# Kernel tuning notes

Measured on AMD Instinct MI355X. Metric: run time of the kernel, lower is better.

## Reference

```python
import jax, jax.numpy as jnp
import numpy as np

OUT_H, OUT_W = 7, 7
SPATIAL_SCALE = 0.25
SAMPLING_RATIO = 2


def setup_inputs() -> dict:
    key = jax.random.key(0)
    k1, k2, k3 = jax.random.split(key, 3)
    x = jax.random.normal(k1, (4, 256, 200, 200), dtype=jnp.float32)
    bidx = jax.random.randint(k2, (1024,), 0, 4).astype(jnp.float32)
    pts = jax.random.uniform(k3, (1024, 4), jnp.float32, 0.0, 800.0)
    x1 = jnp.minimum(pts[:, 0], pts[:, 2])
    x2 = jnp.maximum(pts[:, 0], pts[:, 2])
    y1 = jnp.minimum(pts[:, 1], pts[:, 3])
    y2 = jnp.maximum(pts[:, 1], pts[:, 3])
    rois = jnp.stack([bidx, x1, y1, x2, y2], axis=1)  # [B,5]
    return {"input": x, "rois": rois}


def reference(input, rois):
    feat = input                                  # [N,C,H,W]
    N, C, H, W = feat.shape
    B = rois.shape[0]
    S = SAMPLING_RATIO
    bi = rois[:, 0].astype(jnp.int32)             # [B] batch index (constant)
    boxes = rois[:, 1:] * SPATIAL_SCALE           # xyxy in feature coords
    rx1, ry1, rx2, ry2 = boxes[:, 0], boxes[:, 1], boxes[:, 2], boxes[:, 3]
    roi_w = jnp.maximum(rx2 - rx1, 1.0)
    roi_h = jnp.maximum(ry2 - ry1, 1.0)
    bin_h = roi_h / OUT_H                         # [B]
    bin_w = roi_w / OUT_W

    # per-ROI continuous sample coordinates: [B, OUT_H*S] and [B, OUT_W*S]
    off_h = (jnp.arange(OUT_H, dtype=jnp.float32)[:, None]
             + (jnp.arange(S, dtype=jnp.float32)[None, :] + 0.5) / S).reshape(-1)
    off_w = (jnp.arange(OUT_W, dtype=jnp.float32)[:, None]
             + (jnp.arange(S, dtype=jnp.float32)[None, :] + 0.5) / S).reshape(-1)
    ys = ry1[:, None] + off_h[None, :] * bin_h[:, None]   # [B, Hs]
    xs = rx1[:, None] + off_w[None, :] * bin_w[:, None]   # [B, Ws]

    # bilinear sampling; pixel i's value sits at continuous coordinate i+0.5
    # (this is the "alignment" handled inside point_interpolate)
    py = jnp.clip(ys - 0.5, 0.0, float(H - 1))
    px = jnp.clip(xs - 0.5, 0.0, float(W - 1))
    y0 = jnp.floor(py).astype(jnp.int32)
    x0 = jnp.floor(px).astype(jnp.int32)
    y1i = jnp.minimum(y0 + 1, H - 1)
    x1i = jnp.minimum(x0 + 1, W - 1)
    wy = (py - y0.astype(py.dtype))[:, :, None, None]     # [B,Hs,1,1]
    wx = (px - x0.astype(px.dtype))[:, None, :, None]     # [B,1,Ws,1]

    b = bi[:, None, None]

    def gather(yy, xx):
        # advanced indexing -> [B, Hs, Ws, C]
        return feat[b, :, yy[:, :, None], xx[:, None, :]]

    v = (gather(y0, x0) * (1.0 - wy) * (1.0 - wx)
         + gather(y0, x1i) * (1.0 - wy) * wx
         + gather(y1i, x0) * wy * (1.0 - wx)
         + gather(y1i, x1i) * wy * wx)                    # [B,Hs,Ws,C]

    # average pool the S x S samples within each output bin
    out = v.reshape(B, OUT_H, S, OUT_W, S, C).mean(axis=(2, 4))  # [B,OH,OW,C]
    return out.transpose(0, 3, 1, 2)                             # [B,C,OH,OW]
```

## Files before the change

kernel.cpp:

```cpp
#include <hip/hip_runtime.h>
#include <hip/hip_bf16.h>

#define CC 256
#define HH 200
#define WW 200
#define PLANE (HH * WW)
#define OUT_H 7
#define OUT_W 7
#define NSP   (OUT_H * OUT_W)
#define BMAX  1024

__global__ __launch_bounds__(256) void nchw2nhwc_bf16_sort(
    const float* __restrict__ in, __hip_bfloat16* __restrict__ out,
    const float* __restrict__ rois, int B, unsigned short* __restrict__ perm)
{
    __shared__ float tile[64][65];
    __shared__ unsigned skey[BMAX];

    int n  = blockIdx.z;
    int c0 = blockIdx.y * 64;
    int p0 = blockIdx.x * 64;
    int tx = threadIdx.x & 63;
    int ty = threadIdx.x >> 6;

    const float* src = in + ((size_t)n * CC + c0) * PLANE + p0;
    #pragma unroll
    for (int i = 0; i < 16; ++i) {
        int c = i * 4 + ty;
        tile[c][tx] = src[(size_t)c * PLANE + tx];
    }
    __syncthreads();
    __hip_bfloat16* dst = out + ((size_t)n * PLANE + p0) * CC + c0;
    #pragma unroll
    for (int i = 0; i < 16; ++i) {
        int p = i * 4 + ty;
        dst[(size_t)p * CC + tx] = __float2bfloat16(tile[tx][p]);
    }

    if (blockIdx.x == 0 && blockIdx.y == 0 && blockIdx.z == 0) {
        int t = threadIdx.x;
        for (int i = t; i < BMAX; i += 256) {
            unsigned k = 0xFFFFFFFFu;
            if (i < B) {
                const float* r = rois + i * 5;
                unsigned bi = (unsigned)(int)r[0];
                float cx = (r[1] + r[3]) * 0.125f;
                float cy = (r[2] + r[4]) * 0.125f;
                unsigned ix = (unsigned)fminf(fmaxf(cx, 0.f), 255.f);
                unsigned iy = (unsigned)fminf(fmaxf(cy, 0.f), 255.f);
                unsigned m = 0;
                #pragma unroll
                for (int bp = 0; bp < 8; ++bp) {
                    m |= ((ix >> bp) & 1u) << (2 * bp);
                    m |= ((iy >> bp) & 1u) << (2 * bp + 1);
                }
                k = (bi << 26) | (m << 10) | (unsigned)i;
            }
            skey[i] = k;
        }
        __syncthreads();
        for (int size = 2; size <= BMAX; size <<= 1) {
            for (int stride = size >> 1; stride > 0; stride >>= 1) {
                for (int i = t; i < BMAX; i += 256) {
                    int p = i ^ stride;
                    if (p > i) {
                        bool up = ((i & size) == 0);
                        unsigned a = skey[i], b2 = skey[p];
                        if ((a > b2) == up) { skey[i] = b2; skey[p] = a; }
                    }
                }
                __syncthreads();
            }
        }
        for (int i = t; i < BMAX; i += 256) perm[i] = (unsigned short)(skey[i] & 1023u);
    }
}

__global__ __launch_bounds__(256) void roialign_nhwc2_bf16s(
    const __hip_bfloat16* __restrict__ nhwc,
    const float* __restrict__ rois,
    const unsigned short* __restrict__ perm,
    float* __restrict__ out)
{
    __shared__ float obuf[128 * NSP];
    int nblk = gridDim.x;
    int bid  = blockIdx.x;
    int pos;
    if ((nblk & 7) == 0) { int cpx = nblk >> 3; pos = (bid & 7) * cpx + (bid >> 3); }
    else                 { pos = bid; }
    int slot = pos >> 1;
    int cg   = pos & 1;
    int b    = (int)perm[slot];

    int t  = threadIdx.x;
    int q  = t & 63;
    int wv = t >> 6;

    const float* r = rois + b * 5;
    int   bi  = (int)r[0];
    float rx1 = r[1] * 0.25f, ry1 = r[2] * 0.25f;
    float rx2 = r[3] * 0.25f, ry2 = r[4] * 0.25f;
    float bin_w = fmaxf(rx2 - rx1, 1.0f) * (1.0f / OUT_W);
    float bin_h = fmaxf(ry2 - ry1, 1.0f) * (1.0f / OUT_H);

    const __hip_bfloat16* base = nhwc + (size_t)bi * PLANE * CC + cg * 128 + 2 * q;

    int s0 = wv * 13;
    #pragma unroll
    for (int k = 0; k < 13; ++k) {
        unsigned s = (unsigned)min(s0 + k, NSP - 1);
        unsigned ph = s / 7u, pw = s % 7u;
        float a0 = 0.f, a1 = 0.f;
        #pragma unroll
        for (int iy = 0; iy < 2; ++iy) {
            float yy = ry1 + ((float)ph + ((float)iy + 0.5f) * 0.5f) * bin_h;
            float py = fminf(fmaxf(yy - 0.5f, 0.0f), (float)(HH - 1));
            int   y0 = min((int)py, HH - 2);
            float fy = py - (float)y0;
            #pragma unroll
            for (int ix = 0; ix < 2; ++ix) {
                float xx = rx1 + ((float)pw + ((float)ix + 0.5f) * 0.5f) * bin_w;
                float px = fminf(fmaxf(xx - 0.5f, 0.0f), (float)(WW - 1));
                int   x0 = min((int)px, WW - 2);
                float fx = px - (float)x0;

                const __hip_bfloat16* p00 = base + (size_t)(y0 * WW + x0) * CC;
                unsigned u00 = *(const unsigned*)(p00);
                unsigned u01 = *(const unsigned*)(p00 + CC);
                unsigned u10 = *(const unsigned*)(p00 + WW * CC);
                unsigned u11 = *(const unsigned*)(p00 + WW * CC + CC);

                float w00 = (1.f - fy) * (1.f - fx);
                float w01 = (1.f - fy) * fx;
                float w10 = fy * (1.f - fx);
                float w11 = fy * fx;

                union { unsigned u; float f; } c;
                c.u = u00 << 16;         a0 += c.f * w00;
                c.u = u00 & 0xFFFF0000u; a1 += c.f * w00;
                c.u = u01 << 16;         a0 += c.f * w01;
                c.u = u01 & 0xFFFF0000u; a1 += c.f * w01;
                c.u = u10 << 16;         a0 += c.f * w10;
                c.u = u10 & 0xFFFF0000u; a1 += c.f * w10;
                c.u = u11 << 16;         a0 += c.f * w11;
                c.u = u11 & 0xFFFF0000u; a1 += c.f * w11;
            }
        }
        obuf[(2 * q + 0) * NSP + s] = a0 * 0.25f;
        obuf[(2 * q + 1) * NSP + s] = a1 * 0.25f;
    }
    __syncthreads();

    float* ob = out + (size_t)b * (CC * NSP) + (size_t)cg * (128 * NSP);
    for (int k = t; k < 128 * NSP; k += 256)
        __builtin_nontemporal_store(obuf[k], &ob[k]);
}

__global__ __launch_bounds__(256) void roialign_fallback(
    const float* __restrict__ feat, const float* __restrict__ rois,
    float* __restrict__ out, int total)
{
    int idx = blockIdx.x * blockDim.x + threadIdx.x;
    if (idx >= total) return;
    int pw = idx % OUT_W;
    int ph = (idx / OUT_W) % OUT_H;
    int c  = (idx / NSP) % CC;
    int b  = idx / (NSP * CC);

    const float* r = rois + b * 5;
    int   bi  = (int)r[0];
    float rx1 = r[1] * 0.25f, ry1 = r[2] * 0.25f;
    float rx2 = r[3] * 0.25f, ry2 = r[4] * 0.25f;
    float bin_w = fmaxf(rx2 - rx1, 1.0f) * (1.0f / OUT_W);
    float bin_h = fmaxf(ry2 - ry1, 1.0f) * (1.0f / OUT_H);

    const float* fptr = feat + ((size_t)bi * CC + c) * PLANE;
    float acc = 0.0f;
    #pragma unroll
    for (int iy = 0; iy < 2; ++iy) {
        float yy = ry1 + ((float)ph + ((float)iy + 0.5f) * 0.5f) * bin_h;
        float py = fminf(fmaxf(yy - 0.5f, 0.0f), (float)(HH - 1));
        int   y0 = min((int)py, HH - 2);
        float fy = py - (float)y0;
        #pragma unroll
        for (int ix = 0; ix < 2; ++ix) {
            float xx = rx1 + ((float)pw + ((float)ix + 0.5f) * 0.5f) * bin_w;
            float px = fminf(fmaxf(xx - 0.5f, 0.0f), (float)(WW - 1));
            int   x0 = min((int)px, WW - 2);
            float fx = px - (float)x0;
            const float* p = fptr + y0 * WW + x0;
            acc += p[0]      * (1.f - fy) * (1.f - fx)
                 + p[1]      * (1.f - fy) * fx
                 + p[WW]     * fy * (1.f - fx)
                 + p[WW + 1] * fy * fx;
        }
    }
    out[idx] = acc * 0.25f;
}

extern "C" void kernel_launch(void* const* d_in, const int* in_sizes, int n_in,
                              void* d_out, int out_size, void* d_ws, size_t ws_size,
                              hipStream_t stream) {
    const float* feat = (const float*)d_in[0];
    const float* rois = (const float*)d_in[1];
    float* out = (float*)d_out;

    int N = in_sizes[0] / (CC * PLANE);
    int B = in_sizes[1] / 5;

    size_t nhwc_bytes = (size_t)N * PLANE * CC * sizeof(__hip_bfloat16);
    size_t need = nhwc_bytes + BMAX * sizeof(unsigned short);

    if (ws_size >= need && B <= BMAX) {
        __hip_bfloat16* nhwc = (__hip_bfloat16*)d_ws;
        unsigned short* perm = (unsigned short*)((char*)d_ws + nhwc_bytes);
        nchw2nhwc_bf16_sort<<<dim3(PLANE / 64, CC / 64, N), 256, 0, stream>>>(
            feat, nhwc, rois, B, perm);
        roialign_nhwc2_bf16s<<<dim3(B * 2), 256, 0, stream>>>(nhwc, rois, perm, out);
    } else {
        int total = out_size;
        roialign_fallback<<<(total + 255) / 256, 256, 0, stream>>>(feat, rois, out, total);
    }
}
```

Before: 80.21 us.

## Split transpose and gather into three kernels overlapping per-image work

Replaces the two-kernel flow with three launches. The first transposes images 0 and 1 and builds the sorted ROI permutation plus per-image unit offsets. The second interleaves ROI gathers for images 0 and 1 with the transpose tiles for images 2 and 3, and the third runs the gathers for images 2 and 3. The goal is to overlap the latency-bound gather with the bandwidth-bound transpose, at the cost of an extra launch and shared-memory sizing for the larger of the two roles. The fast path now requires exactly 1024 ROIs and 4 images.

Result: slower. 114.7 us (+43.0%).

```diff
diff --git a/kernel.cpp b/kernel.cpp
--- a/kernel.cpp
+++ b/kernel.cpp
@@ -8,20 +8,19 @@
 #define OUT_H 7
 #define OUT_W 7
 #define NSP   (OUT_H * OUT_W)
-#define BMAX  1024
-
-__global__ __launch_bounds__(256) void nchw2nhwc_bf16_sort(
-    const float* __restrict__ in, __hip_bfloat16* __restrict__ out,
-    const float* __restrict__ rois, int B, unsigned short* __restrict__ perm)
-{
-    __shared__ float tile[64][65];
-    __shared__ unsigned skey[BMAX];
-
-    int n  = blockIdx.z;
-    int c0 = blockIdx.y * 64;
-    int p0 = blockIdx.x * 64;
-    int tx = threadIdx.x & 63;
-    int ty = threadIdx.x >> 6;
+#define NIMG  4
+#define NB    1024
+#define TPI   2500
+#define SHBYTES 25088
+
+__device__ __forceinline__ void transpose_tile(
+    const float* __restrict__ in, __hip_bfloat16* __restrict__ nhwc,
+    char* shraw, int n, int t, int tid)
+{
+    float (*tile)[65] = (float(*)[65])shraw;
+    int c0 = (t / 625) * 64;
+    int p0 = (t % 625) * 64;
+    int tx = tid & 63, ty = tid >> 6;
 
     const float* src = in + ((size_t)n * CC + c0) * PLANE + p0;
     #pragma unroll
@@ -30,71 +29,25 @@
         tile[c][tx] = src[(size_t)c * PLANE + tx];
     }
     __syncthreads();
-    __hip_bfloat16* dst = out + ((size_t)n * PLANE + p0) * CC + c0;
+    __hip_bfloat16* dst = nhwc + ((size_t)n * PLANE + p0) * CC + c0;
     #pragma unroll
     for (int i = 0; i < 16; ++i) {
         int p = i * 4 + ty;
         dst[(size_t)p * CC + tx] = __float2bfloat16(tile[tx][p]);
     }
-
-    if (blockIdx.x == 0 && blockIdx.y == 0 && blockIdx.z == 0) {
-        int t = threadIdx.x;
-        for (int i = t; i < BMAX; i += 256) {
-            unsigned k = 0xFFFFFFFFu;
-            if (i < B) {
-                const float* r = rois + i * 5;
-                unsigned bi = (unsigned)(int)r[0];
-                float cx = (r[1] + r[3]) * 0.125f;
-                float cy = (r[2] + r[4]) * 0.125f;
-                unsigned ix = (unsigned)fminf(fmaxf(cx, 0.f), 255.f);
-                unsigned iy = (unsigned)fminf(fmaxf(cy, 0.f), 255.f);
-                unsigned m = 0;
-                #pragma unroll
-                for (int bp = 0; bp < 8; ++bp) {
-                    m |= ((ix >> bp) & 1u) << (2 * bp);
-                    m |= ((iy >> bp) & 1u) << (2 * bp + 1);
-                }
-                k = (bi << 26) | (m << 10) | (unsigned)i;
-            }
-            skey[i] = k;
-        }
-        __syncthreads();
-        for (int size = 2; size <= BMAX; size <<= 1) {
-            for (int stride = size >> 1; stride > 0; stride >>= 1) {
-                for (int i = t; i < BMAX; i += 256) {
-                    int p = i ^ stride;
-                    if (p > i) {
-                        bool up = ((i & size) == 0);
-                        unsigned a = skey[i], b2 = skey[p];
-                        if ((a > b2) == up) { skey[i] = b2; skey[p] = a; }
-                    }
-                }
-                __syncthreads();
-            }
-        }
-        for (int i = t; i < BMAX; i += 256) perm[i] = (unsigned short)(skey[i] & 1023u);
-    }
-}
-
-__global__ __launch_bounds__(256) void roialign_nhwc2_bf16s(
-    const __hip_bfloat16* __restrict__ nhwc,
-    const float* __restrict__ rois,
-    const unsigned short* __restrict__ perm,
-    float* __restrict__ out)
-{
-    __shared__ float obuf[128 * NSP];
-    int nblk = gridDim.x;
-    int bid  = blockIdx.x;
-    int pos;
-    if ((nblk & 7) == 0) { int cpx = nblk >> 3; pos = (bid & 7) * cpx + (bid >> 3); }
-    else                 { pos = bid; }
-    int slot = pos >> 1;
-    int cg   = pos & 1;
+}
+
+__device__ __forceinline__ void gather_unit(
+    const __hip_bfloat16* __restrict__ nhwc, const float* __restrict__ rois,
+    const unsigned short* __restrict__ perm, float* __restrict__ out,
+    char* shraw, int u, int tid)
+{
+    float* obuf = (float*)shraw;
+    int slot = u >> 1;
+    int cg   = u & 1;
     int b    = (int)perm[slot];
-
-    int t  = threadIdx.x;
-    int q  = t & 63;
-    int wv = t >> 6;
+    int q    = tid & 63;
+    int wv   = tid >> 6;
 
     const float* r = rois + b * 5;
     int   bi  = (int)r[0];
@@ -135,15 +88,15 @@
                 float w10 = fy * (1.f - fx);
                 float w11 = fy * fx;
 
-                union { unsigned u; float f; } c;
-                c.u = u00 << 16;         a0 += c.f * w00;
-                c.u = u00 & 0xFFFF0000u; a1 += c.f * w00;
-                c.u = u01 << 16;         a0 += c.f * w01;
-                c.u = u01 & 0xFFFF0000u; a1 += c.f * w01;
-                c.u = u10 << 16;         a0 += c.f * w10;
-                c.u = u10 & 0xFFFF0000u; a1 += c.f * w10;
-                c.u = u11 << 16;         a0 += c.f * w11;
-                c.u = u11 & 0xFFFF0000u; a1 += c.f * w11;
+                union { unsigned uu; float f; } c;
+                c.uu = u00 << 16;         a0 += c.f * w00;
+                c.uu = u00 & 0xFFFF0000u; a1 += c.f * w00;
+                c.uu = u01 << 16;         a0 += c.f * w01;
+                c.uu = u01 & 0xFFFF0000u; a1 += c.f * w01;
+                c.uu = u10 << 16;         a0 += c.f * w10;
+                c.uu = u10 & 0xFFFF0000u; a1 += c.f * w10;
+                c.uu = u11 << 16;         a0 += c.f * w11;
+                c.uu = u11 & 0xFFFF0000u; a1 += c.f * w11;
             }
         }
         obuf[(2 * q + 0) * NSP + s] = a0 * 0.25f;
@@ -152,8 +105,95 @@
     __syncthreads();
 
     float* ob = out + (size_t)b * (CC * NSP) + (size_t)cg * (128 * NSP);
-    for (int k = t; k < 128 * NSP; k += 256)
+    for (int k = tid; k < 128 * NSP; k += 256)
         __builtin_nontemporal_store(obuf[k], &ob[k]);
+}
+
+__global__ __launch_bounds__(256) void k1_trans01_sort(
+    const float* __restrict__ in, __hip_bfloat16* __restrict__ nhwc,
+    const float* __restrict__ rois, unsigned short* __restrict__ perm,
+    int* __restrict__ ustart)
+{
+    __shared__ char shraw[SHBYTES] __attribute__((aligned(16)));
+    __shared__ int hist[NIMG];
+    int bid = blockIdx.x, tid = threadIdx.x;
+
+    if (bid < 2 * TPI) {
+        transpose_tile(in, nhwc, shraw, bid / TPI, bid % TPI, tid);
+        return;
+    }
+
+    unsigned* skey = (unsigned*)shraw;
+    if (tid < NIMG) hist[tid] = 0;
+    __syncthreads();
+    for (int i = tid; i < NB; i += 256) {
+        const float* r = rois + i * 5;
+        unsigned bi2 = (unsigned)(int)r[0];
+        atomicAdd(&hist[bi2], 1);
+        float cx = (r[1] + r[3]) * 0.125f;
+        float cy = (r[2] + r[4]) * 0.125f;
+        unsigned ix = (unsigned)fminf(fmaxf(cx, 0.f), 255.f);
+        unsigned iy = (unsigned)fminf(fmaxf(cy, 0.f), 255.f);
+        unsigned m = 0;
+        #pragma unroll
+        for (int bp = 0; bp < 8; ++bp) {
+            m |= ((ix >> bp) & 1u) << (2 * bp);
+            m |= ((iy >> bp) & 1u) << (2 * bp + 1);
+        }
+        skey[i] = (bi2 << 26) | (m << 10) | (unsigned)i;
+    }
+    __syncthreads();
+    for (int size = 2; size <= NB; size <<= 1) {
+        for (int stride = size >> 1; stride > 0; stride >>= 1) {
+            for (int i = tid; i < NB; i += 256) {
+                int p = i ^ stride;
+                if (p > i) {
+                    bool up = ((i & size) == 0);
+                    unsigned a = skey[i], b2 = skey[p];
+                    if ((a > b2) == up) { skey[i] = b2; skey[p] = a; }
+                }
+            }
+            __syncthreads();
+        }
+    }
+    for (int i = tid; i < NB; i += 256) perm[i] = (unsigned short)(skey[i] & 1023u);
+    if (tid == 0) {
+        int c = 0;
+        #pragma unroll
+        for (int im = 0; im < NIMG; ++im) { ustart[im] = 2 * c; c += hist[im]; }
+        ustart[NIMG] = 2 * c;
+    }
+}
+
+__global__ __launch_bounds__(256) void k2_mixed(
+    const float* __restrict__ in, __hip_bfloat16* __restrict__ nhwc,
+    const float* __restrict__ rois, const unsigned short* __restrict__ perm,
+    const int* __restrict__ ustart, float* __restrict__ out)
+{
+    __shared__ char shraw[SHBYTES] __attribute__((aligned(16)));
+    int bid = blockIdx.x, tid = threadIdx.x;
+    int g = bid / 7, r = bid % 7;
+
+    if (r < 2) {
+        int u = g * 2 + r;
+        if (u < ustart[2])
+            gather_unit(nhwc, rois, perm, out, shraw, u, tid);
+    } else {
+        int t = g * 5 + (r - 2);
+        if (t < 2 * TPI)
+            transpose_tile(in, nhwc, shraw, 2 + t / TPI, t % TPI, tid);
+    }
+}
+
+__global__ __launch_bounds__(256) void k3_gather23(
+    const __hip_bfloat16* __restrict__ nhwc, const float* __restrict__ rois,
+    const unsigned short* __restrict__ perm, const int* __restrict__ ustart,
+    float* __restrict__ out)
+{
+    __shared__ char shraw[SHBYTES] __attribute__((aligned(16)));
+    int u = ustart[2] + blockIdx.x;
+    if (u < ustart[4])
+        gather_unit(nhwc, rois, perm, out, shraw, u, threadIdx.x);
 }
 
 __global__ __launch_bounds__(256) void roialign_fallback(
@@ -209,14 +249,17 @@
     int B = in_sizes[1] / 5;
 
     size_t nhwc_bytes = (size_t)N * PLANE * CC * sizeof(__hip_bfloat16);
-    size_t need = nhwc_bytes + BMAX * sizeof(unsigned short);
-
-    if (ws_size >= need && B <= BMAX) {
+    size_t perm_off   = nhwc_bytes;
+    size_t us_off     = nhwc_bytes + NB * sizeof(unsigned short);
+    size_t need       = us_off + (NIMG + 1) * sizeof(int);
+
+    if (ws_size >= need && B == NB && N == NIMG) {
         __hip_bfloat16* nhwc = (__hip_bfloat16*)d_ws;
-        unsigned short* perm = (unsigned short*)((char*)d_ws + nhwc_bytes);
-        nchw2nhwc_bf16_sort<<<dim3(PLANE / 64, CC / 64, N), 256, 0, stream>>>(
-            feat, nhwc, rois, B, perm);
-        roialign_nhwc2_bf16s<<<dim3(B * 2), 256, 0, stream>>>(nhwc, rois, perm, out);
+        unsigned short* perm = (unsigned short*)((char*)d_ws + perm_off);
+        int*            us   = (int*)((char*)d_ws + us_off);
+        k1_trans01_sort<<<dim3(2 * TPI + 1), 256, 0, stream>>>(feat, nhwc, rois, perm, us);
+        k2_mixed<<<dim3(7 * 1024), 256, 0, stream>>>(feat, nhwc, rois, perm, us, out);
+        k3_gather23<<<dim3(2 * NB), 256, 0, stream>>>(nhwc, rois, perm, us, out);
     } else {
         int total = out_size;
         roialign_fallback<<<(total + 255) / 256, 256, 0, stream>>>(feat, rois, out, total);
```
